# Kernel tuning notes

Hardware: AMD Instinct MI355X
Metric: run time of the kernel (lower is better)

## Reference

```python
import math
import jax, jax.numpy as jnp
import numpy as np

EMBED_DIM = 1024
NUM_HEADS = 16
HEAD_DIM = EMBED_DIM // NUM_HEADS


def setup_inputs() -> dict:
    key = jax.random.key(0)
    kx, kqkv, kproj = jax.random.split(key, 3)
    b, sq, h = 2, 2048, EMBED_DIM
    x = jax.random.normal(kx, (b, sq, h), dtype=jnp.float32)
    # torch Linear weights are [out_features, in_features]
    # xavier_uniform for qkv: bound = sqrt(6/(fan_in+fan_out))
    bound_qkv = math.sqrt(6.0 / (h + 3 * h))
    Wqkv = jax.random.uniform(kqkv, (3 * h, h), dtype=jnp.float32,
                              minval=-bound_qkv, maxval=bound_qkv)
    # kaiming_uniform(a=sqrt(5)) for proj: bound = 1/sqrt(fan_in)
    bound_p = 1.0 / math.sqrt(h)
    Wproj = jax.random.uniform(kproj, (h, h), dtype=jnp.float32,
                               minval=-bound_p, maxval=bound_p)
    bproj = jnp.zeros((h,), dtype=jnp.float32)
    # self-attention: query == key == value (module asserts equality)
    return {"query": x, "key": x, "value": x,
            "Wqkv": Wqkv, "Wproj": Wproj, "bproj": bproj}


def reference(query, key, value, Wqkv, Wproj, bproj):
    b, sq, h = query.shape
    nh, hn = NUM_HEADS, HEAD_DIM
    # permute to [sq, b, h] then flatten tokens (seq-major)
    x = jnp.transpose(query, (1, 0, 2)).reshape(sq * b, h)
    qkv = x @ Wqkv.T                       # [sq*b, 3h] (no qkv bias: add_bias_kv=False)
    qkv = qkv.reshape(sq, b, nh, 3 * hn)
    q, k, v = jnp.split(qkv, 3, axis=-1)   # each [sq, b, nh, hn]
    # view to (sq, b*nh, hn) then transpose(0,1) -> [b*nh, sq, hn] (b-major, nh-minor)
    q = q.reshape(sq, b * nh, hn).transpose(1, 0, 2)
    k = k.reshape(sq, b * nh, hn).transpose(1, 0, 2)
    v = v.reshape(sq, b * nh, hn).transpose(1, 0, 2)
    scale = 1.0 / math.sqrt(hn)
    scores = jnp.einsum('nqd,nkd->nqk', q, k) * scale   # [b*nh, sq, sq] full matrix
    attn = jax.nn.softmax(scores, axis=-1)
    ctx = jnp.einsum('nqk,nkd->nqd', attn, v)           # [b*nh, sq, hn]
    # NOTE: original code views the b*nh (b-major) dim as (nh, b) -- reproduce exactly
    ctx = ctx.reshape(nh, b, sq, hn)
    ctx = jnp.transpose(ctx, (2, 1, 0, 3)).reshape(sq * b, h)
    out = ctx @ Wproj.T + bproj
    out = out.reshape(sq, b, h)
    return jnp.transpose(out, (1, 0, 2))   # [b, sq, h]
```

## Files before the change

kernel.cpp:

```cpp
#include <hip/hip_runtime.h>
#include <stdint.h>

#define B_   2
#define SQ   2048
#define H    1024
#define NH   16
#define HN   64
#define T_TOK 4096
#define N3H  3072

typedef __bf16 bf16x8 __attribute__((ext_vector_type(8)));
typedef float  f32x4  __attribute__((ext_vector_type(4)));

#define MFMA16(a, b, c) __builtin_amdgcn_mfma_f32_16x16x32_bf16((a), (b), (c), 0, 0, 0)

#define LGKM_DRAIN() do { \
  __builtin_amdgcn_s_waitcnt(0xC07F); \
  __builtin_amdgcn_wave_barrier(); \
} while (0)

__device__ __forceinline__ uint16_t f2bf_u(float f) {
  union { float f; uint32_t u; } v; v.f = f;
  uint32_t u = v.u;
  u += 0x7fffu + ((u >> 16) & 1u);
  return (uint16_t)(u >> 16);
}

__device__ __forceinline__ bf16x8 ldb8(const uint16_t* p) {
  return *reinterpret_cast<const bf16x8*>(p);
}

__device__ __forceinline__ void gll16(const uint16_t* g, uint16_t* l) {
  __builtin_amdgcn_global_load_lds(
      (const __attribute__((address_space(1))) uint32_t*)g,
      (__attribute__((address_space(3))) uint32_t*)l, 16, 0, 0);
}

__global__ __launch_bounds__(256) void convert_kernel(
    const float* __restrict__ x, const float* __restrict__ wqkv,
    const float* __restrict__ wproj,
    uint16_t* __restrict__ xb, uint16_t* __restrict__ wqkvb,
    uint16_t* __restrict__ wprojb) {
  const int XT4 = (T_TOK * H) / 4;
  const int WQ4 = (N3H * H) / 4;
  int i4 = blockIdx.x * 256 + threadIdx.x;
  const float* src;
  uint16_t* dst;
  if (i4 < XT4) {
    int i = i4 * 4;
    int t = i >> 10, c = i & 1023;
    int bi = t & 1, s = t >> 1;
    src = x + (bi * SQ + s) * H + c;
    dst = xb + i;
  } else if (i4 < XT4 + WQ4) {
    int j = (i4 - XT4) * 4;
    src = wqkv + j; dst = wqkvb + j;
  } else {
    int j = (i4 - XT4 - WQ4) * 4;
    src = wproj + j; dst = wprojb + j;
  }
  float4 v = *(const float4*)src;
  ushort4 o;
  o.x = f2bf_u(v.x); o.y = f2bf_u(v.y); o.z = f2bf_u(v.z); o.w = f2bf_u(v.w);
  *(ushort4*)dst = o;
}

__global__ __launch_bounds__(256) void gemm_qkv_kernel(
    const uint16_t* __restrict__ xb, const uint16_t* __restrict__ wb,
    uint16_t* __restrict__ Qb, uint16_t* __restrict__ Kb,
    uint16_t* __restrict__ Vtb) {
  const int lane = threadIdx.x & 63;
  const int wave = threadIdx.x >> 6;
  const int quad = lane >> 4, l16 = lane & 15;
  const int wm = wave >> 1, wn = wave & 1;
  const int row0 = blockIdx.y * 128, col0 = blockIdx.x * 128;

  __shared__ __align__(16) char smem[4 * 64 * 76 * 2];
  uint16_t* sA = (uint16_t*)smem;
  uint16_t* sB = (uint16_t*)(smem + 8192);
  uint16_t* W  = (uint16_t*)(smem) + wave * (64 * 76);

  const int lrow = lane >> 2;
  const int lk   = (lane & 3) * 8;

  f32x4 acc[4][4];
#pragma unroll
  for (int i = 0; i < 4; ++i)
#pragma unroll
    for (int j = 0; j < 4; ++j) acc[i][j] = (f32x4){0.f, 0.f, 0.f, 0.f};

  for (int k0 = 0; k0 < H; k0 += 32) {
#pragma unroll
    for (int c = 0; c < 2; ++c) {
      int g = c * 4 + wave;
      gll16(xb + (size_t)(row0 + g * 16 + lrow) * H + k0 + lk, sA + g * 512);
      gll16(wb + (size_t)(col0 + g * 16 + lrow) * H + k0 + lk, sB + g * 512);
    }
    __syncthreads();
    bf16x8 af[4], bfr[4];
#pragma unroll
    for (int mt = 0; mt < 4; ++mt)
      af[mt] = ldb8(sA + (wm * 64 + mt * 16 + l16) * 32 + quad * 8);
#pragma unroll
    for (int nt = 0; nt < 4; ++nt)
      bfr[nt] = ldb8(sB + (wn * 64 + nt * 16 + l16) * 32 + quad * 8);
#pragma unroll
    for (int mt = 0; mt < 4; ++mt)
#pragma unroll
      for (int nt = 0; nt < 4; ++nt)
        acc[mt][nt] = MFMA16(af[mt], bfr[nt], acc[mt][nt]);
    __syncthreads();
  }

  const int c0 = col0 + wn * 64;
  const int cm = c0 >> 6;
  const int hd = cm / 3;
  const int which = cm - hd * 3;
  const int t0 = row0 + wm * 64;

  if (which < 2) {
#pragma unroll
    for (int mt = 0; mt < 4; ++mt)
#pragma unroll
      for (int nt = 0; nt < 4; ++nt)
#pragma unroll
        for (int r = 0; r < 4; ++r)
          W[(mt * 16 + quad * 4 + r) * 76 + nt * 16 + l16] = f2bf_u(acc[mt][nt][r]);
    LGKM_DRAIN();
    uint16_t* dstb = (which == 0) ? Qb : Kb;
    const int t8 = lane >> 3, d0 = (lane & 7) * 8;
#pragma unroll
    for (int it = 0; it < 8; ++it) {
      int tl = it * 8 + t8;
      int t = t0 + tl;
      int s = t >> 1;
      int n = (t & 1) * NH + hd;
      bf16x8 vv = ldb8(W + tl * 76 + d0);
      *(bf16x8*)(dstb + (size_t)(n * SQ + s) * HN + d0) = vv;
    }
  } else {
    uint32_t* W32 = (uint32_t*)W;
#pragma unroll
    for (int mt = 0; mt < 4; ++mt)
#pragma unroll
      for (int nt = 0; nt < 4; ++nt) {
        int base = (nt * 16 + l16) * 76 + mt * 8 + quad * 2;
        W32[base >> 1] =
            (uint32_t)f2bf_u(acc[mt][nt][0]) | ((uint32_t)f2bf_u(acc[mt][nt][2]) << 16);
        W32[(base >> 1) + 16] =
            (uint32_t)f2bf_u(acc[mt][nt][1]) | ((uint32_t)f2bf_u(acc[mt][nt][3]) << 16);
      }
    LGKM_DRAIN();
    const int dl = lane >> 3;
    const int bi = (lane >> 2) & 1;
    const int sc = (lane & 3) * 8;
    const int s0 = (row0 >> 1) + wm * 32;
    const int n = bi * NH + hd;
#pragma unroll
    for (int it = 0; it < 8; ++it) {
      int d = it * 8 + dl;
      bf16x8 vv = ldb8(W + d * 76 + bi * 32 + sc);
      *(bf16x8*)(Vtb + (size_t)(n * HN + d) * SQ + s0 + sc) = vv;
    }
  }
}

__global__ __launch_bounds__(512, 6) void attn_kernel(
    const uint16_t* __restrict__ Qb, const uint16_t* __restrict__ Kb,
    const uint16_t* __restrict__ Vtb, uint16_t* __restrict__ ctxb) {
  const int lane = threadIdx.x & 63;
  const int wave = threadIdx.x >> 6;
  const int quad = lane >> 4, l16 = lane & 15;
  const int head  = blockIdx.x;
  const int qtile = blockIdx.y;
  const int wq = wave & 3;
  const int hf = wave >> 2;
  const int q0 = qtile * 64 + wq * 16;

  const uint16_t* Qh = Qb + (size_t)head * SQ * HN;
  const uint16_t* Kh = Kb + (size_t)head * SQ * HN;
  const uint16_t* Vh = Vtb + (size_t)head * HN * SQ;

  __shared__ __align__(16) char smem_raw[51200];
  uint16_t (*stage)[2][64][64] = (uint16_t(*)[2][64][64])smem_raw;
  float (*cacc)[64][21]        = (float(*)[64][21])smem_raw;
  uint16_t (*plds)[16][72]     = (uint16_t(*)[16][72])(smem_raw + 32768);

  const int lr8 = lane >> 3;
  const int lc8 = lane & 7;
  const int sc8 = (lc8 - lr8) & 7;

  bf16x8 aq0 = ldb8(Qh + (q0 + l16) * HN + quad * 8);
  bf16x8 aq1 = ldb8(Qh + (q0 + l16) * HN + 32 + quad * 8);

  float lrun[4];
  f32x4 acc[4];
#pragma unroll
  for (int r = 0; r < 4; ++r) {
    lrun[r] = 0.f;
    acc[r] = (f32x4){0.f, 0.f, 0.f, 0.f};
  }
  const float sc2 = 0.125f * 1.44269504f;

  for (int kt = 0; kt < 16; ++kt) {
    const int kbase = (hf * 16 + kt) * 64;
#pragma unroll
    for (int j = 0; j < 2; ++j) {
      int rr = wq * 16 + j * 8;
      gll16(Kh + (size_t)(kbase + rr + lr8) * HN + sc8 * 8, &stage[hf][0][rr][0]);
      gll16(Vh + (size_t)(rr + lr8) * SQ + kbase + sc8 * 8, &stage[hf][1][rr][0]);
    }
    __syncthreads();

    f32x4 s4[4];
#pragma unroll
    for (int st = 0; st < 4; ++st) {
      bf16x8 k0 = ldb8(&stage[hf][0][st * 16 + l16][0] + ((quad + l16) & 7) * 8);
      bf16x8 k1 = ldb8(&stage[hf][0][st * 16 + l16][0] + ((quad + 4 + l16) & 7) * 8);
      f32x4 z = (f32x4){0.f, 0.f, 0.f, 0.f};
      z = MFMA16(aq0, k0, z);
      s4[st] = MFMA16(aq1, k1, z);
    }
#pragma unroll
    for (int st = 0; st < 4; ++st)
#pragma unroll
      for (int r = 0; r < 4; ++r) {
        float p = __builtin_amdgcn_exp2f(s4[st][r] * sc2);
        plds[wave][quad * 4 + r][st * 16 + l16] = f2bf_u(p);
        lrun[r] += p;
      }
    LGKM_DRAIN();
    bf16x8 ap0 = ldb8(&plds[wave][l16][quad * 8]);
    bf16x8 ap1 = ldb8(&plds[wave][l16][32 + quad * 8]);
#pragma unroll
    for (int dt = 0; dt < 4; ++dt) {
      bf16x8 v0 = ldb8(&stage[hf][1][dt * 16 + l16][0] + ((quad + l16) & 7) * 8);
      bf16x8 v1 = ldb8(&stage[hf][1][dt * 16 + l16][0] + ((quad + 4 + l16) & 7) * 8);
      acc[dt] = MFMA16(ap0, v0, acc[dt]);
      acc[dt] = MFMA16(ap1, v1, acc[dt]);
    }
    __syncthreads();
  }

  if (hf) {
    float* dst = cacc[wq][lane];
#pragma unroll
    for (int dt = 0; dt < 4; ++dt)
#pragma unroll
      for (int r = 0; r < 4; ++r) dst[dt * 4 + r] = acc[dt][r];
#pragma unroll
    for (int r = 0; r < 4; ++r) dst[16 + r] = lrun[r];
  }
  __syncthreads();
  if (hf) return;
  {
    const float* src = cacc[wq][lane];
#pragma unroll
    for (int dt = 0; dt < 4; ++dt)
#pragma unroll
      for (int r = 0; r < 4; ++r) acc[dt][r] += src[dt * 4 + r];
#pragma unroll
    for (int r = 0; r < 4; ++r) lrun[r] += src[16 + r];
  }

  float rinv[4];
#pragma unroll
  for (int r = 0; r < 4; ++r) {
    float ls = lrun[r];
    ls += __shfl_xor(ls, 1);
    ls += __shfl_xor(ls, 2);
    ls += __shfl_xor(ls, 4);
    ls += __shfl_xor(ls, 8);
    rinv[r] = __builtin_amdgcn_rcpf(ls);
  }
#pragma unroll
  for (int dt = 0; dt < 4; ++dt)
#pragma unroll
    for (int r = 0; r < 4; ++r)
      plds[wave][quad * 4 + r][dt * 16 + l16] = f2bf_u(acc[dt][r] * rinv[r]);
  LGKM_DRAIN();
  {
    const int q8 = lane >> 3, d0 = (lane & 7) * 8;
    const int gc = (head >> 1) * HN + d0;
#pragma unroll
    for (int it = 0; it < 2; ++it) {
      int ql = it * 8 + q8;
      bf16x8 vv = ldb8(&plds[wave][ql][d0]);
      int row = 2 * (q0 + ql) + (head & 1);
      *(bf16x8*)(ctxb + (size_t)row * H + gc) = vv;
    }
  }
}

__global__ __launch_bounds__(256) void gemm_proj_kernel(
    const uint16_t* __restrict__ ab, const uint16_t* __restrict__ wb,
    const float* __restrict__ bias, float* __restrict__ out) {
  const int lane = threadIdx.x & 63;
  const int wave = threadIdx.x >> 6;
  const int quad = lane >> 4, l16 = lane & 15;
  const int row0 = blockIdx.y * 128, col0 = blockIdx.x * 64;

  __shared__ __align__(16) uint16_t sA[128 * 32];
  __shared__ __align__(16) uint16_t sB[64 * 32];

  const int lrow = lane >> 2;
  const int lk   = (lane & 3) * 8;

  f32x4 acc[2][4];
#pragma unroll
  for (int i = 0; i < 2; ++i)
#pragma unroll
    for (int j = 0; j < 4; ++j) acc[i][j] = (f32x4){0.f, 0.f, 0.f, 0.f};

  for (int k0 = 0; k0 < H; k0 += 32) {
#pragma unroll
    for (int c = 0; c < 2; ++c) {
      int g = c * 4 + wave;
      gll16(ab + (size_t)(row0 + g * 16 + lrow) * H + k0 + lk, sA + g * 512);
    }
    gll16(wb + (size_t)(col0 + wave * 16 + lrow) * H + k0 + lk, sB + wave * 512);
    __syncthreads();
    bf16x8 af[2], bfr[4];
#pragma unroll
    for (int mt = 0; mt < 2; ++mt)
      af[mt] = ldb8(sA + (wave * 32 + mt * 16 + l16) * 32 + quad * 8);
#pragma unroll
    for (int nt = 0; nt < 4; ++nt)
      bfr[nt] = ldb8(sB + (nt * 16 + l16) * 32 + quad * 8);
#pragma unroll
    for (int mt = 0; mt < 2; ++mt)
#pragma unroll
      for (int nt = 0; nt < 4; ++nt)
        acc[mt][nt] = MFMA16(af[mt], bfr[nt], acc[mt][nt]);
    __syncthreads();
  }

#pragma unroll
  for (int mt = 0; mt < 2; ++mt)
#pragma unroll
    for (int nt = 0; nt < 4; ++nt)
#pragma unroll
      for (int r = 0; r < 4; ++r) {
        int m = row0 + wave * 32 + mt * 16 + quad * 4 + r;
        int c = col0 + nt * 16 + l16;
        int s = m >> 1, bi = m & 1;
        out[(size_t)(bi * SQ + s) * H + c] = acc[mt][nt][r] + bias[c];
      }
}

extern "C" void kernel_launch(void* const* d_in, const int* in_sizes, int n_in,
                              void* d_out, int out_size, void* d_ws, size_t ws_size,
                              hipStream_t stream) {
  const float* x     = (const float*)d_in[0];
  const float* wqkv  = (const float*)d_in[3];
  const float* wproj = (const float*)d_in[4];
  const float* bproj = (const float*)d_in[5];
  float* out = (float*)d_out;

  char* ws = (char*)d_ws;
  uint16_t* xb     = (uint16_t*)(ws);
  uint16_t* wqkvb  = (uint16_t*)(ws + (8ull  << 20));
  uint16_t* wprojb = (uint16_t*)(ws + (14ull << 20));
  uint16_t* Qb     = (uint16_t*)(ws + (16ull << 20));
  uint16_t* Kb     = (uint16_t*)(ws + (24ull << 20));
  uint16_t* Vtb    = (uint16_t*)(ws + (32ull << 20));
  uint16_t* ctxb   = (uint16_t*)(ws + (40ull << 20));

  convert_kernel<<<8192, 256, 0, stream>>>(x, wqkv, wproj, xb, wqkvb, wprojb);
  gemm_qkv_kernel<<<dim3(N3H / 128, T_TOK / 128), 256, 0, stream>>>(xb, wqkvb, Qb, Kb, Vtb);
  attn_kernel<<<dim3(B_ * NH, SQ / 64), 512, 0, stream>>>(Qb, Kb, Vtb, ctxb);
  gemm_proj_kernel<<<dim3(H / 64, T_TOK / 128), 256, 0, stream>>>(ctxb, wprojb, bproj, out);
}
```

Measured before the change: 229.1 us.

## Rewrite attention with 32x32 MFMA, register-resident P, double buffering, XCD-aware mapping

The attention kernel now uses 32x32x16 MFMA with a transposed S=K·Q formulation, so each wave handles 32 query rows and the probability tile stays in registers via lane shuffles instead of an LDS round trip. K/V tiles are double-buffered so global-to-LDS loads for the next tile overlap compute, and a flat grid of 512 blocks maps four heads to each XCD for L2 reuse. The row-sum is accumulated from bf16-rounded probabilities. Per-block work doubles, the grid halves, LDS use grows to 64KB, and the occupancy target drops from 6 to 4.

```diff
diff --git a/kernel.cpp b/kernel.cpp
--- a/kernel.cpp
+++ b/kernel.cpp
@@ -11,8 +11,10 @@
 
 typedef __bf16 bf16x8 __attribute__((ext_vector_type(8)));
 typedef float  f32x4  __attribute__((ext_vector_type(4)));
+typedef float  f32x16 __attribute__((ext_vector_type(16)));
 
 #define MFMA16(a, b, c) __builtin_amdgcn_mfma_f32_16x16x32_bf16((a), (b), (c), 0, 0, 0)
+#define MFMA32(a, b, c) __builtin_amdgcn_mfma_f32_32x32x16_bf16((a), (b), (c), 0, 0, 0)
 
 #define LGKM_DRAIN() do { \
   __builtin_amdgcn_s_waitcnt(0xC07F); \
@@ -24,6 +26,14 @@
   uint32_t u = v.u;
   u += 0x7fffu + ((u >> 16) & 1u);
   return (uint16_t)(u >> 16);
+}
+
+__device__ __forceinline__ uint32_t cvtpk2(float a, float b, float* sum) {
+  union { __bf16 h[2]; uint32_t u; } r;
+  r.h[0] = (__bf16)a;
+  r.h[1] = (__bf16)b;
+  *sum += (float)r.h[0] + (float)r.h[1];
+  return r.u;
 }
 
 __device__ __forceinline__ bf16x8 ldb8(const uint16_t* p) {
@@ -165,129 +175,149 @@
   }
 }
 
-__global__ __launch_bounds__(512, 6) void attn_kernel(
+__global__ __launch_bounds__(512, 4) void attn_kernel(
     const uint16_t* __restrict__ Qb, const uint16_t* __restrict__ Kb,
     const uint16_t* __restrict__ Vtb, uint16_t* __restrict__ ctxb) {
   const int lane = threadIdx.x & 63;
   const int wave = threadIdx.x >> 6;
-  const int quad = lane >> 4, l16 = lane & 15;
-  const int head  = blockIdx.x;
-  const int qtile = blockIdx.y;
+  const int l32 = lane & 31;
+  const int hi  = lane >> 5;
   const int wq = wave & 3;
   const int hf = wave >> 2;
-  const int q0 = qtile * 64 + wq * 16;
+
+  const int bid = blockIdx.x;
+  const int xcd = bid & 7, slot = bid >> 3;
+  const int head = xcd * 4 + (slot >> 4);
+  const int qt   = slot & 15;
+  const int q0w  = qt * 128 + wq * 32;
 
   const uint16_t* Qh = Qb + (size_t)head * SQ * HN;
   const uint16_t* Kh = Kb + (size_t)head * SQ * HN;
   const uint16_t* Vh = Vtb + (size_t)head * HN * SQ;
 
-  __shared__ __align__(16) char smem_raw[51200];
-  uint16_t (*stage)[2][64][64] = (uint16_t(*)[2][64][64])smem_raw;
-  float (*cacc)[64][21]        = (float(*)[64][21])smem_raw;
-  uint16_t (*plds)[16][72]     = (uint16_t(*)[16][72])(smem_raw + 32768);
-
-  const int lr8 = lane >> 3;
-  const int lc8 = lane & 7;
+  __shared__ __align__(16) char smem[65536];
+  float (*cacc)[64][33] = (float(*)[64][33])smem;
+  uint16_t* ctile = (uint16_t*)(smem + 36864) + wq * (32 * 72);
+
+  const int lr8 = lane >> 3, lc8 = lane & 7;
   const int sc8 = (lc8 - lr8) & 7;
 
-  bf16x8 aq0 = ldb8(Qh + (q0 + l16) * HN + quad * 8);
-  bf16x8 aq1 = ldb8(Qh + (q0 + l16) * HN + 32 + quad * 8);
-
-  float lrun[4];
-  f32x4 acc[4];
-#pragma unroll
-  for (int r = 0; r < 4; ++r) {
-    lrun[r] = 0.f;
-    acc[r] = (f32x4){0.f, 0.f, 0.f, 0.f};
-  }
+  bf16x8 qf[4];
+#pragma unroll
+  for (int dc = 0; dc < 4; ++dc)
+    qf[dc] = ldb8(Qh + (size_t)(q0w + l32) * HN + dc * 16 + hi * 8);
+
+  f32x16 acc[2];
+#pragma unroll
+  for (int dt = 0; dt < 2; ++dt)
+#pragma unroll
+    for (int e = 0; e < 16; ++e) acc[dt][e] = 0.f;
+  float lrun = 0.f;
   const float sc2 = 0.125f * 1.44269504f;
 
-  for (int kt = 0; kt < 16; ++kt) {
+  auto STAGE = [&](int b, int kt) {
+    uint16_t* sK = (uint16_t*)(smem + hf * 32768 + b * 16384);
+    uint16_t* sV = sK + 4096;
     const int kbase = (hf * 16 + kt) * 64;
 #pragma unroll
     for (int j = 0; j < 2; ++j) {
       int rr = wq * 16 + j * 8;
-      gll16(Kh + (size_t)(kbase + rr + lr8) * HN + sc8 * 8, &stage[hf][0][rr][0]);
-      gll16(Vh + (size_t)(rr + lr8) * SQ + kbase + sc8 * 8, &stage[hf][1][rr][0]);
+      gll16(Kh + (size_t)(kbase + rr + lr8) * HN + sc8 * 8, sK + rr * 64);
+      gll16(Vh + (size_t)(rr + lr8) * SQ + kbase + sc8 * 8, sV + rr * 64);
+    }
+  };
+
+  STAGE(0, 0);
+  __syncthreads();
+
+#pragma unroll 2
+  for (int kt = 0; kt < 16; ++kt) {
+    const int cur = kt & 1;
+    if (kt < 15) STAGE(cur ^ 1, kt + 1);
+    const uint16_t* sK = (const uint16_t*)(smem + hf * 32768 + cur * 16384);
+    const uint16_t* sV = sK + 4096;
+
+#pragma unroll
+    for (int ktile = 0; ktile < 2; ++ktile) {
+      f32x16 s;
+#pragma unroll
+      for (int e = 0; e < 16; ++e) s[e] = 0.f;
+#pragma unroll
+      for (int dc = 0; dc < 4; ++dc) {
+        bf16x8 kf = ldb8(sK + (ktile * 32 + l32) * 64 + ((dc * 2 + hi + l32) & 7) * 8);
+        s = MFMA32(kf, qf[dc], s);
+      }
+      uint32_t c[8];
+#pragma unroll
+      for (int i = 0; i < 8; ++i) {
+        float p0 = __builtin_amdgcn_exp2f(s[2 * i] * sc2);
+        float p1 = __builtin_amdgcn_exp2f(s[2 * i + 1] * sc2);
+        c[i] = cvtpk2(p0, p1, &lrun);
+      }
+      uint32_t w[8];
+#pragma unroll
+      for (int g = 0; g < 2; ++g)
+#pragma unroll
+        for (int x = 0; x < 2; ++x) {
+          uint32_t a  = c[g * 4 + x];
+          uint32_t bb = c[g * 4 + 2 + x];
+          uint32_t ta = (uint32_t)__shfl_xor((int)a, 32);
+          uint32_t tb = (uint32_t)__shfl_xor((int)bb, 32);
+          w[g * 4 + x]     = hi ? tb : a;
+          w[g * 4 + 2 + x] = hi ? bb : ta;
+        }
+      union { uint32_t u[4]; bf16x8 v; } pa0, pa1;
+#pragma unroll
+      for (int x = 0; x < 4; ++x) { pa0.u[x] = w[x]; pa1.u[x] = w[4 + x]; }
+#pragma unroll
+      for (int dt = 0; dt < 2; ++dt) {
+        bf16x8 v0 = ldb8(sV + (dt * 32 + l32) * 64 + ((ktile * 4 + 0 + hi + l32) & 7) * 8);
+        bf16x8 v1 = ldb8(sV + (dt * 32 + l32) * 64 + ((ktile * 4 + 2 + hi + l32) & 7) * 8);
+        acc[dt] = MFMA32(pa0.v, v0, acc[dt]);
+        acc[dt] = MFMA32(pa1.v, v1, acc[dt]);
+      }
     }
     __syncthreads();
-
-    f32x4 s4[4];
-#pragma unroll
-    for (int st = 0; st < 4; ++st) {
-      bf16x8 k0 = ldb8(&stage[hf][0][st * 16 + l16][0] + ((quad + l16) & 7) * 8);
-      bf16x8 k1 = ldb8(&stage[hf][0][st * 16 + l16][0] + ((quad + 4 + l16) & 7) * 8);
-      f32x4 z = (f32x4){0.f, 0.f, 0.f, 0.f};
-      z = MFMA16(aq0, k0, z);
-      s4[st] = MFMA16(aq1, k1, z);
-    }
-#pragma unroll
-    for (int st = 0; st < 4; ++st)
-#pragma unroll
-      for (int r = 0; r < 4; ++r) {
-        float p = __builtin_amdgcn_exp2f(s4[st][r] * sc2);
-        plds[wave][quad * 4 + r][st * 16 + l16] = f2bf_u(p);
-        lrun[r] += p;
-      }
-    LGKM_DRAIN();
-    bf16x8 ap0 = ldb8(&plds[wave][l16][quad * 8]);
-    bf16x8 ap1 = ldb8(&plds[wave][l16][32 + quad * 8]);
-#pragma unroll
-    for (int dt = 0; dt < 4; ++dt) {
-      bf16x8 v0 = ldb8(&stage[hf][1][dt * 16 + l16][0] + ((quad + l16) & 7) * 8);
-      bf16x8 v1 = ldb8(&stage[hf][1][dt * 16 + l16][0] + ((quad + 4 + l16) & 7) * 8);
-      acc[dt] = MFMA16(ap0, v0, acc[dt]);
-      acc[dt] = MFMA16(ap1, v1, acc[dt]);
-    }
-    __syncthreads();
   }
 
   if (hf) {
-    float* dst = cacc[wq][lane];
-#pragma unroll
-    for (int dt = 0; dt < 4; ++dt)
-#pragma unroll
-      for (int r = 0; r < 4; ++r) dst[dt * 4 + r] = acc[dt][r];
-#pragma unroll
-    for (int r = 0; r < 4; ++r) dst[16 + r] = lrun[r];
+    float* dst = &cacc[wq][lane][0];
+#pragma unroll
+    for (int dt = 0; dt < 2; ++dt)
+#pragma unroll
+      for (int e = 0; e < 16; ++e) dst[dt * 16 + e] = acc[dt][e];
+    dst[32] = lrun;
   }
   __syncthreads();
   if (hf) return;
   {
-    const float* src = cacc[wq][lane];
-#pragma unroll
-    for (int dt = 0; dt < 4; ++dt)
-#pragma unroll
-      for (int r = 0; r < 4; ++r) acc[dt][r] += src[dt * 4 + r];
-#pragma unroll
-    for (int r = 0; r < 4; ++r) lrun[r] += src[16 + r];
-  }
-
-  float rinv[4];
-#pragma unroll
-  for (int r = 0; r < 4; ++r) {
-    float ls = lrun[r];
-    ls += __shfl_xor(ls, 1);
-    ls += __shfl_xor(ls, 2);
-    ls += __shfl_xor(ls, 4);
-    ls += __shfl_xor(ls, 8);
-    rinv[r] = __builtin_amdgcn_rcpf(ls);
-  }
-#pragma unroll
-  for (int dt = 0; dt < 4; ++dt)
-#pragma unroll
-    for (int r = 0; r < 4; ++r)
-      plds[wave][quad * 4 + r][dt * 16 + l16] = f2bf_u(acc[dt][r] * rinv[r]);
+    const float* src = &cacc[wq][lane][0];
+#pragma unroll
+    for (int dt = 0; dt < 2; ++dt)
+#pragma unroll
+      for (int e = 0; e < 16; ++e) acc[dt][e] += src[dt * 16 + e];
+    lrun += src[32];
+  }
+
+  float ls = lrun + __shfl_xor(lrun, 32);
+  float rinv = __builtin_amdgcn_rcpf(ls);
+#pragma unroll
+  for (int e = 0; e < 16; ++e) {
+    int qe = (e & 3) + 8 * (e >> 2) + 4 * hi;
+    float rv = __shfl(rinv, qe);
+    ctile[qe * 72 + l32]      = f2bf_u(acc[0][e] * rv);
+    ctile[qe * 72 + 32 + l32] = f2bf_u(acc[1][e] * rv);
+  }
   LGKM_DRAIN();
   {
     const int q8 = lane >> 3, d0 = (lane & 7) * 8;
-    const int gc = (head >> 1) * HN + d0;
-#pragma unroll
-    for (int it = 0; it < 2; ++it) {
+    const int gcb = (head >> 1) * HN;
+#pragma unroll
+    for (int it = 0; it < 4; ++it) {
       int ql = it * 8 + q8;
-      bf16x8 vv = ldb8(&plds[wave][ql][d0]);
-      int row = 2 * (q0 + ql) + (head & 1);
-      *(bf16x8*)(ctxb + (size_t)row * H + gc) = vv;
+      bf16x8 vv = ldb8(ctile + ql * 72 + d0);
+      int row = 2 * (q0w + ql) + (head & 1);
+      *(bf16x8*)(ctxb + (size_t)row * H + gcb + d0) = vv;
     }
   }
 }
@@ -368,6 +398,6 @@
 
   convert_kernel<<<8192, 256, 0, stream>>>(x, wqkv, wproj, xb, wqkvb, wprojb);
   gemm_qkv_kernel<<<dim3(N3H / 128, T_TOK / 128), 256, 0, stream>>>(xb, wqkvb, Qb, Kb, Vtb);
-  attn_kernel<<<dim3(B_ * NH, SQ / 64), 512, 0, stream>>>(Qb, Kb, Vtb, ctxb);
+  attn_kernel<<<512, 512, 0, stream>>>(Qb, Kb, Vtb, ctxb);
   gemm_proj_kernel<<<dim3(H / 64, T_TOK / 128), 256, 0, stream>>>(ctxb, wprojb, bproj, out);
 }
```

After: 216.3 us. 5.6% less time.
